# Performance work log

Measured on AMD Instinct MI355X. Metric: run time of the kernel, lower is better.

## Reference

```python
import jax, jax.numpy as jnp
import numpy as np

B, Nq, C = 1, 40000, 256
Hh, L, P = 8, 4, 8
hd = C // Hh
LEVEL_SHAPES = [(128, 128), (64, 64), (32, 32), (16, 16)]


def setup_inputs() -> dict:
    key = jax.random.key(0)
    ks = jax.random.split(key, 16)
    inp = {}
    inp['query'] = jax.random.normal(ks[0], (B, Nq, C), jnp.float32)
    # reference points in [-1, 1] normalized coords (x, y)
    inp['reference_points'] = jax.random.uniform(ks[1], (B, Nq, L, 2), jnp.float32) * 2.0 - 1.0
    for i, (h, w) in enumerate(LEVEL_SHAPES):
        inp[f'feat{i}'] = jax.random.normal(ks[2 + i], (B, C, h, w), jnp.float32)
    # learned params (torch Linear y = x @ W + b, W stored as [in, out])
    inp['W_off'] = jax.random.normal(ks[6], (C, Hh * L * P * 2), jnp.float32) * 0.02
    inp['b_off'] = jax.random.normal(ks[7], (Hh * L * P * 2,), jnp.float32) * 0.5
    inp['W_attn'] = jax.random.normal(ks[8], (C, Hh * L * P), jnp.float32) * 0.02
    inp['b_attn'] = jnp.zeros((Hh * L * P,), jnp.float32)
    inp['W_val'] = jax.random.normal(ks[9], (C, C), jnp.float32) * (1.0 / np.sqrt(C))
    inp['b_val'] = jnp.zeros((C,), jnp.float32)
    inp['W_out'] = jax.random.normal(ks[10], (C, C), jnp.float32) * (1.0 / np.sqrt(C))
    inp['b_out'] = jnp.zeros((C,), jnp.float32)
    return inp


def _deform_sample(v, coords):
    # Bilinear grid_sample, align_corners=True, zeros padding.
    # v: [B, Hh, H, W, hd]; coords: [B, Hh, S, 2] in [-1, 1] (x, y)
    _, _, H, W, _ = v.shape
    x = (coords[..., 0] + 1.0) * 0.5 * (W - 1)
    y = (coords[..., 1] + 1.0) * 0.5 * (H - 1)
    x0 = jnp.floor(x)
    y0 = jnp.floor(y)
    vflat = v.reshape(v.shape[0], v.shape[1], H * W, v.shape[4])

    def corner(xi, yi, w):
        inb = (xi >= 0) & (xi <= W - 1) & (yi >= 0) & (yi <= H - 1)
        idx = (jnp.clip(yi, 0, H - 1) * W + jnp.clip(xi, 0, W - 1)).astype(jnp.int32)
        g = jnp.take_along_axis(vflat, idx[..., None], axis=2)  # [B,Hh,S,hd]
        return g * (w * inb)[..., None]

    return (corner(x0, y0, (x0 + 1 - x) * (y0 + 1 - y))
            + corner(x0 + 1, y0, (x - x0) * (y0 + 1 - y))
            + corner(x0, y0 + 1, (x0 + 1 - x) * (y - y0))
            + corner(x0 + 1, y0 + 1, (x - x0) * (y - y0)))


def reference(query, feat0, feat1, feat2, feat3, reference_points,
              W_off, b_off, W_attn, b_attn, W_val, b_val, W_out, b_out):
    feats = [feat0, feat1, feat2, feat3]
    off = (query @ W_off + b_off).reshape(B, Nq, Hh, L, P, 2)
    w = (query @ W_attn + b_attn).reshape(B, Nq, Hh, L, P)
    w = jax.nn.softmax(w, axis=-1)  # softmax over points, per level
    # samp: [B, Nq, Hh, L, P, 2]
    samp = reference_points[:, :, None, :, None, :] + jnp.tanh(off) * 0.25

    out = jnp.zeros((B, Nq, Hh, hd), jnp.float32)
    for l, f in enumerate(feats):
        Hl, Wl = f.shape[2], f.shape[3]
        v = jnp.einsum('bchw,cd->bhwd', f, W_val) + b_val  # value proj
        v = v.reshape(B, Hl, Wl, Hh, hd).transpose(0, 3, 1, 2, 4)  # [B,Hh,H,W,hd]
        coords = samp[:, :, :, l].transpose(0, 2, 1, 3, 4).reshape(B, Hh, Nq * P, 2)
        s = _deform_sample(v, coords).reshape(B, Hh, Nq, P, hd)
        wl = w[:, :, :, l].transpose(0, 2, 1, 3)  # [B,Hh,Nq,P]
        out = out + jnp.einsum('bhnpd,bhnp->bnhd', s, wl)

    return out.reshape(B, Nq, C) @ W_out + b_out
```

## Files before the change

### kernel.cpp

```cpp
#include <hip/hip_runtime.h>
#include <hip/hip_fp16.h>
#include <math.h>

#define NQ 40000

typedef short s16x8 __attribute__((ext_vector_type(8)));
typedef float f32x4 __attribute__((ext_vector_type(4)));

static constexpr int HLa[4] = {128, 64, 32, 16};
static constexpr int HWa[4] = {16384, 4096, 1024, 256};
static constexpr int VB[4] = {0, 4194304, 5242880, 5505024};

__device__ __forceinline__ short bf16hi(float x) {
    union { float f; unsigned u; } v; v.f = x;
    unsigned r = v.u + 0x7FFFu + ((v.u >> 16) & 1u);
    return (short)(r >> 16);
}
__device__ __forceinline__ float bf16f(short s) {
    union { unsigned u; float f; } v; v.u = ((unsigned)(unsigned short)s) << 16;
    return v.f;
}
__device__ __forceinline__ float fast_tanh(float x) {
    float xc = fminf(fmaxf(x, -15.f), 15.f);
    float e = __expf(2.f * xc);
    return (e - 1.f) / (e + 1.f);
}
#define MFMA16(a, b, c) __builtin_amdgcn_mfma_f32_16x16x32_bf16(a, b, c, 0, 0, 0)

__global__ __launch_bounds__(256) void prep_w(
    const float* __restrict__ Woff, const float* __restrict__ Wattn,
    const float* __restrict__ Wout, short* __restrict__ WtH, short* __restrict__ WtL)
{
    int r = blockIdx.x, c = threadIdx.x;
    float x;
    if (r < 512)      x = Woff[c * 512 + r];
    else if (r < 768) x = Wattn[c * 256 + (r - 512)];
    else              x = Wout[c * 256 + (r - 768)];
    short hi = bf16hi(x);
    WtH[r * 256 + c] = hi;
    WtL[r * 256 + c] = bf16hi(x - bf16f(hi));
}

__global__ __launch_bounds__(256) void vproj_kernel(
    const float* __restrict__ f0, const float* __restrict__ f1,
    const float* __restrict__ f2, const float* __restrict__ f3,
    const float* __restrict__ Wv, const float* __restrict__ bv,
    __half* __restrict__ v)
{
    __shared__ float fT[256 * 16];

    int bid = blockIdx.x;
    const float* f;
    int base, HWl, hw0;
    if (bid < 1024)      { f = f0; base = VB[0]; HWl = 16384; hw0 = bid * 16; }
    else if (bid < 1280) { f = f1; base = VB[1]; HWl = 4096;  hw0 = (bid - 1024) * 16; }
    else if (bid < 1344) { f = f2; base = VB[2]; HWl = 1024;  hw0 = (bid - 1280) * 16; }
    else                 { f = f3; base = VB[3]; HWl = 256;   hw0 = (bid - 1344) * 16; }

    int t = threadIdx.x;
    for (int k = 0; k < 16; ++k) {
        int idx = k * 256 + t;
        int c = idx >> 4, j = idx & 15;
        fT[idx] = f[c * HWl + hw0 + j];
    }
    __syncthreads();

    int to4 = (t & 63) * 4;
    int hw4 = (t >> 6) * 4;

    float4 bv4 = *(const float4*)(bv + to4);
    float acc[4][4];
    #pragma unroll
    for (int i = 0; i < 4; ++i) {
        acc[i][0] = bv4.x; acc[i][1] = bv4.y; acc[i][2] = bv4.z; acc[i][3] = bv4.w;
    }

    #pragma unroll 4
    for (int c = 0; c < 256; ++c) {
        float4 w4 = *(const float4*)(Wv + c * 256 + to4);
        float4 fv = *(const float4*)(fT + c * 16 + hw4);
        float fa[4] = {fv.x, fv.y, fv.z, fv.w};
        float wa[4] = {w4.x, w4.y, w4.z, w4.w};
        #pragma unroll
        for (int i = 0; i < 4; ++i)
            #pragma unroll
            for (int j = 0; j < 4; ++j)
                acc[i][j] += fa[i] * wa[j];
    }

    int hh = to4 >> 5, dd4 = to4 & 31;
    #pragma unroll
    for (int i = 0; i < 4; ++i) {
        int hw = hw0 + hw4 + i;
        __half2 h0 = __floats2half2_rn(acc[i][0], acc[i][1]);
        __half2 h1 = __floats2half2_rn(acc[i][2], acc[i][3]);
        uint2 st = make_uint2(*(unsigned*)&h0, *(unsigned*)&h1);
        *(uint2*)(v + base + (hh * HWl + hw) * 32 + dd4) = st;
    }
}

__global__ __launch_bounds__(256, 5) void msda_kernel(
    const float* __restrict__ query, const float* __restrict__ refp,
    const float* __restrict__ boff,  const float* __restrict__ battn,
    const float* __restrict__ bout,
    const short* __restrict__ WtH,   const short* __restrict__ WtL,
    const __half* __restrict__ v,    float* __restrict__ out)
{
    __shared__ __align__(16) char lds[29952];
    short*    sQh  = (short*)lds;
    short*    sQl  = (short*)(lds + 8448);
    float*    offL = (float*)lds;
    uint2*    sPWh = (uint2*)(lds + 8448);
    __half*   sWh  = (__half*)(lds + 16896);
    unsigned* sPI  = (unsigned*)(lds + 25344);
    float*    sR   = (float*)(lds + 29440);

    const int t = threadIdx.x;
    const int n0 = blockIdx.x * 16;
    const int wv = t >> 6, lane = t & 63;
    const int mrow = lane & 15, kg = lane >> 4;

    for (int k2 = 0; k2 < 16; ++k2) {
        float x = query[(n0 + k2) * 256 + t];
        short hi = bf16hi(x);
        sQh[k2 * 264 + t] = hi;
        sQl[k2 * 264 + t] = bf16hi(x - bf16f(hi));
    }
    if (t < 128) sR[t] = refp[n0 * 8 + t];
    __syncthreads();

    f32x4 accO[8], accA[4];
    {
        f32x4 z = {0.f, 0.f, 0.f, 0.f};
        #pragma unroll
        for (int j = 0; j < 8; ++j) accO[j] = z;
        #pragma unroll
        for (int j = 0; j < 4; ++j) accA[j] = z;
    }
    {
        const short* offH = WtH + (wv * 128 + mrow) * 256 + kg * 8;
        const short* offLo = WtL + (wv * 128 + mrow) * 256 + kg * 8;
        const short* attH = WtH + (512 + wv * 64 + mrow) * 256 + kg * 8;
        const short* attL = WtL + (512 + wv * 64 + mrow) * 256 + kg * 8;
        const int aoff = mrow * 264 + kg * 8;
        #pragma unroll
        for (int kk = 0; kk < 8; ++kk) {
            s16x8 ah = *(const s16x8*)(sQh + aoff + kk * 32);
            s16x8 al = *(const s16x8*)(sQl + aoff + kk * 32);
            #pragma unroll
            for (int j = 0; j < 8; ++j) {
                s16x8 bh = *(const s16x8*)(offH + j * 4096 + kk * 32);
                s16x8 bl = *(const s16x8*)(offLo + j * 4096 + kk * 32);
                accO[j] = MFMA16(ah, bh, accO[j]);
                accO[j] = MFMA16(al, bh, accO[j]);
                accO[j] = MFMA16(ah, bl, accO[j]);
            }
            #pragma unroll
            for (int ja = 0; ja < 4; ++ja) {
                s16x8 bh = *(const s16x8*)(attH + ja * 4096 + kk * 32);
                s16x8 bl = *(const s16x8*)(attL + ja * 4096 + kk * 32);
                accA[ja] = MFMA16(ah, bh, accA[ja]);
                accA[ja] = MFMA16(al, bh, accA[ja]);
                accA[ja] = MFMA16(ah, bl, accA[ja]);
            }
        }
    }
    #pragma unroll
    for (int j = 0; j < 8; ++j) {
        float bb = boff[wv * 128 + j * 16 + mrow];
        #pragma unroll
        for (int r = 0; r < 4; ++r) accO[j][r] += bb;
    }
    #pragma unroll
    for (int ja = 0; ja < 4; ++ja) {
        float bb = battn[wv * 64 + ja * 16 + mrow];
        #pragma unroll
        for (int r = 0; r < 4; ++r) accA[ja][r] += bb;
    }

    #pragma unroll
    for (int ja = 0; ja < 4; ++ja) {
        int hh = 2 * wv + (ja >> 1);
        int l  = ((ja & 1) << 1) | (mrow >> 3);
        int p  = mrow & 7;
        #pragma unroll
        for (int r = 0; r < 4; ++r) {
            float x = accA[ja][r];
            float m = fmaxf(x, __shfl_xor(x, 1));
            m = fmaxf(m, __shfl_xor(m, 2));
            m = fmaxf(m, __shfl_xor(m, 4));
            float e = __expf(x - m);
            float s = e + __shfl_xor(e, 1);
            s += __shfl_xor(s, 2);
            s += __shfl_xor(s, 4);
            int q = kg * 4 + r;
            sWh[q * 264 + hh * 32 + l * 8 + p] = __float2half_rn(e / s);
        }
    }
    __syncthreads();

    const int dd2 = t & 15, hhpS = (t >> 4) & 1, qp = t >> 5;

    for (int k = 0; k < 4; ++k) {
        if (wv == k) {
            #pragma unroll
            for (int j = 0; j < 8; ++j)
                #pragma unroll
                for (int r = 0; r < 4; ++r)
                    offL[(kg * 4 + r) * 132 + j * 16 + mrow] = accO[j][r];
        }
        __syncthreads();

        #pragma unroll
        for (int it = 0; it < 4; ++it) {
            int s = it * 256 + t;
            int q = s >> 6, hhL = (s >> 5) & 1, l = (s >> 3) & 3, p = s & 7;
            const int Wl = 128 >> l;
            const float scl = 0.5f * (float)(Wl - 1);
            float lx = offL[q * 132 + hhL * 64 + l * 16 + p * 2];
            float ly = offL[q * 132 + hhL * 64 + l * 16 + p * 2 + 1];
            float w  = __half2float(sWh[q * 264 + (2 * k + hhL) * 32 + l * 8 + p]);
            float rx = sR[q * 8 + l * 2], ry = sR[q * 8 + l * 2 + 1];
            float cx = rx + fast_tanh(lx) * 0.25f;
            float cy = ry + fast_tanh(ly) * 0.25f;
            float xx = (cx + 1.f) * scl, yy = (cy + 1.f) * scl;
            float x0f = floorf(xx), y0f = floorf(yy);
            float fx = xx - x0f, fy = yy - y0f;
            int x0 = (int)x0f, y0 = (int)y0f;
            int xc0 = min(max(x0, 0), Wl - 1);
            int xc1 = min(max(x0 + 1, 0), Wl - 1);
            int yc0 = min(max(y0, 0), Wl - 1);
            int yc1 = min(max(y0 + 1, 0), Wl - 1);
            bool bx0 = (x0 >= 0) & (x0 < Wl);
            bool bx1 = (x0 + 1 >= 0) & (x0 + 1 < Wl);
            bool by0 = (y0 >= 0) & (y0 < Wl);
            bool by1 = (y0 + 1 >= 0) & (y0 + 1 < Wl);
            float w00 = (bx0 && by0) ? (1.f - fx) * (1.f - fy) * w : 0.f;
            float w01 = (bx1 && by0) ? fx * (1.f - fy) * w : 0.f;
            float w10 = (bx0 && by1) ? (1.f - fx) * fy * w : 0.f;
            float w11 = (bx1 && by1) ? fx * fy * w : 0.f;
            unsigned pw = (unsigned)(yc0 * Wl + xc0)
                        | ((unsigned)(xc1 - xc0) << 14)
                        | ((unsigned)(yc1 - yc0) << 15);
            sPI[s] = pw;
            __half2 hA = __floats2half2_rn(w00, w01);
            __half2 hB = __floats2half2_rn(w10, w11);
            sPWh[s] = make_uint2(*(unsigned*)&hA, *(unsigned*)&hB);
        }
        __syncthreads();

        {
            const int hh = 2 * k + hhpS;
            #pragma unroll
            for (int qi2 = 0; qi2 < 2; ++qi2) {
                int qi = qp * 2 + qi2;
                float accx = 0.f, accy = 0.f;
                #pragma unroll
                for (int l = 0; l < 4; ++l) {
                    const int Wl = HLa[l];
                    const __half2* vl = (const __half2*)(v + VB[l] + hh * HWa[l] * 32 + dd2 * 2);
                    int sbase = ((qi * 2 + hhpS) * 4 + l) * 8;
                    #pragma unroll
                    for (int p = 0; p < 8; ++p) {
                        unsigned pw = sPI[sbase + p];
                        uint2 ww = sPWh[sbase + p];
                        float2 fa = __half22float2(*(__half2*)&ww.x);
                        float2 fb = __half22float2(*(__half2*)&ww.y);
                        int idx = pw & 0x3FFF;
                        int dxo = ((pw >> 14) & 1) * 16;
                        int dyo = ((pw >> 15) & 1) * (Wl * 16);
                        const __half2* b00 = vl + idx * 16;
                        float2 f00 = __half22float2(b00[0]);
                        float2 f01 = __half22float2(b00[dxo]);
                        float2 f10 = __half22float2(b00[dyo]);
                        float2 f11 = __half22float2(b00[dxo + dyo]);
                        accx += fa.x * f00.x + fa.y * f01.x + fb.x * f10.x + fb.y * f11.x;
                        accy += fa.x * f00.y + fa.y * f01.y + fb.x * f10.y + fb.y * f11.y;
                    }
                }
                *(__half2*)(sWh + qi * 264 + hh * 32 + dd2 * 2) =
                    __floats2half2_rn(accx, accy);
            }
        }
        __syncthreads();
    }

    {
        int q = t & 15, seg = t >> 4;
        const __half2* src = (const __half2*)(sWh + q * 264 + seg * 16);
        short* dh = sQh + q * 264 + seg * 16;
        short* dl = sQl + q * 264 + seg * 16;
        #pragma unroll
        for (int jj = 0; jj < 8; ++jj) {
            float2 f = __half22float2(src[jj]);
            short h0 = bf16hi(f.x), h1 = bf16hi(f.y);
            dh[2 * jj]     = h0;
            dh[2 * jj + 1] = h1;
            dl[2 * jj]     = bf16hi(f.x - bf16f(h0));
            dl[2 * jj + 1] = bf16hi(f.y - bf16f(h1));
        }
    }
    __syncthreads();

    {
        f32x4 accE[4];
        f32x4 z = {0.f, 0.f, 0.f, 0.f};
        #pragma unroll
        for (int e = 0; e < 4; ++e) accE[e] = z;
        const short* outH = WtH + (768 + wv * 64 + mrow) * 256 + kg * 8;
        const short* outL = WtL + (768 + wv * 64 + mrow) * 256 + kg * 8;
        const int aoff = mrow * 264 + kg * 8;
        #pragma unroll
        for (int kk = 0; kk < 8; ++kk) {
            s16x8 ah = *(const s16x8*)(sQh + aoff + kk * 32);
            s16x8 al = *(const s16x8*)(sQl + aoff + kk * 32);
            #pragma unroll
            for (int e = 0; e < 4; ++e) {
                s16x8 bh = *(const s16x8*)(outH + e * 4096 + kk * 32);
                s16x8 bl = *(const s16x8*)(outL + e * 4096 + kk * 32);
                accE[e] = MFMA16(ah, bh, accE[e]);
                accE[e] = MFMA16(al, bh, accE[e]);
                accE[e] = MFMA16(ah, bl, accE[e]);
            }
        }
        #pragma unroll
        for (int e = 0; e < 4; ++e) {
            int col = wv * 64 + e * 16 + mrow;
            float bb = bout[col];
            #pragma unroll
            for (int r = 0; r < 4; ++r)
                out[(n0 + kg * 4 + r) * 256 + col] = accE[e][r] + bb;
        }
    }
}

extern "C" void kernel_launch(void* const* d_in, const int* in_sizes, int n_in,
                              void* d_out, int out_size, void* d_ws, size_t ws_size,
                              hipStream_t stream) {
    const float* query = (const float*)d_in[0];
    const float* refp  = (const float*)d_in[1];
    const float* f0    = (const float*)d_in[2];
    const float* f1    = (const float*)d_in[3];
    const float* f2    = (const float*)d_in[4];
    const float* f3    = (const float*)d_in[5];
    const float* Woff  = (const float*)d_in[6];
    const float* boff  = (const float*)d_in[7];
    const float* Wattn = (const float*)d_in[8];
    const float* battn = (const float*)d_in[9];
    const float* Wval  = (const float*)d_in[10];
    const float* bval  = (const float*)d_in[11];
    const float* Wout  = (const float*)d_in[12];
    const float* bout  = (const float*)d_in[13];

    __half* v  = (__half*)d_ws;
    short* WtH = (short*)((char*)d_ws + 11141120);
    short* WtL = WtH + 262144;
    float* outp = (float*)d_out;

    prep_w<<<1024, 256, 0, stream>>>(Woff, Wattn, Wout, WtH, WtL);
    vproj_kernel<<<1360, 256, 0, stream>>>(f0, f1, f2, f3, Wval, bval, v);
    msda_kernel<<<2500, 256, 0, stream>>>(query, refp, boff, battn, bout,
                                          WtH, WtL, v, outp);
}
```

Before: 572.2 us.

## Make sampling stage wave-local to remove block-wide barriers per head pair

Restructures the deformable sampling phase so each wave handles its own two heads across all 16 queries, using per-wave LDS scratch for offsets and sample records. This replaces the four-iteration loop with block-wide __syncthreads by wave-local lgkmcnt waits, and splits levels across lane groups with a shuffle reduction. LDS use grows from about 30KB to about 54KB, so the launch bound drops from 5 to 3 blocks per SM, which lowers occupancy for this latency-bound gather.

```diff
diff --git a/kernel.cpp b/kernel.cpp
--- a/kernel.cpp
+++ b/kernel.cpp
@@ -99,26 +99,27 @@
     }
 }
 
-__global__ __launch_bounds__(256, 5) void msda_kernel(
+__global__ __launch_bounds__(256, 3) void msda_kernel(
     const float* __restrict__ query, const float* __restrict__ refp,
     const float* __restrict__ boff,  const float* __restrict__ battn,
     const float* __restrict__ bout,
     const short* __restrict__ WtH,   const short* __restrict__ WtL,
     const __half* __restrict__ v,    float* __restrict__ out)
 {
-    __shared__ __align__(16) char lds[29952];
+    __shared__ __align__(16) char lds[54272];
     short*    sQh  = (short*)lds;
     short*    sQl  = (short*)(lds + 8448);
-    float*    offL = (float*)lds;
-    uint2*    sPWh = (uint2*)(lds + 8448);
-    __half*   sWh  = (__half*)(lds + 16896);
-    unsigned* sPI  = (unsigned*)(lds + 25344);
-    float*    sR   = (float*)(lds + 29440);
+    __half*   preT = (__half*)(lds + 33792);
+    __half*   sWh  = (__half*)(lds + 42240);
+    float*    sR   = (float*)(lds + 53760);
 
     const int t = threadIdx.x;
     const int n0 = blockIdx.x * 16;
     const int wv = t >> 6, lane = t & 63;
     const int mrow = lane & 15, kg = lane >> 4;
+    float*    offW = (float*)lds + wv * 2112;
+    unsigned* sPIw = (unsigned*)(lds + 50688 + wv * 768);
+    uint2*    sPWw = (uint2*)(lds + 50688 + wv * 768 + 256);
 
     for (int k2 = 0; k2 < 16; ++k2) {
         float x = query[(n0 + k2) * 256 + t];
@@ -177,6 +178,13 @@
         #pragma unroll
         for (int r = 0; r < 4; ++r) accA[ja][r] += bb;
     }
+    __syncthreads();
+
+    #pragma unroll
+    for (int j = 0; j < 8; ++j)
+        #pragma unroll
+        for (int r = 0; r < 4; ++r)
+            offW[(kg * 4 + r) * 132 + j * 16 + mrow] = accO[j][r];
 
     #pragma unroll
     for (int ja = 0; ja < 4; ++ja) {
@@ -197,97 +205,93 @@
             sWh[q * 264 + hh * 32 + l * 8 + p] = __float2half_rn(e / s);
         }
     }
-    __syncthreads();
-
-    const int dd2 = t & 15, hhpS = (t >> 4) & 1, qp = t >> 5;
-
-    for (int k = 0; k < 4; ++k) {
-        if (wv == k) {
-            #pragma unroll
-            for (int j = 0; j < 8; ++j)
-                #pragma unroll
-                for (int r = 0; r < 4; ++r)
-                    offL[(kg * 4 + r) * 132 + j * 16 + mrow] = accO[j][r];
-        }
-        __syncthreads();
-
-        #pragma unroll
-        for (int it = 0; it < 4; ++it) {
-            int s = it * 256 + t;
-            int q = s >> 6, hhL = (s >> 5) & 1, l = (s >> 3) & 3, p = s & 7;
-            const int Wl = 128 >> l;
-            const float scl = 0.5f * (float)(Wl - 1);
-            float lx = offL[q * 132 + hhL * 64 + l * 16 + p * 2];
-            float ly = offL[q * 132 + hhL * 64 + l * 16 + p * 2 + 1];
-            float w  = __half2float(sWh[q * 264 + (2 * k + hhL) * 32 + l * 8 + p]);
-            float rx = sR[q * 8 + l * 2], ry = sR[q * 8 + l * 2 + 1];
+    asm volatile("s_waitcnt lgkmcnt(0)" ::: "memory");
+    __builtin_amdgcn_sched_barrier(0);
+
+    const int l_p = (lane >> 3) & 3, p_p = lane & 7, hhL_p = lane >> 5;
+    const int Wl_p = 128 >> l_p;
+    const float scl_p = 0.5f * (float)(Wl_p - 1);
+    const int whCol = (2 * wv + hhL_p) * 32 + l_p * 8 + p_p;
+    const int sg = kg, ch2 = mrow;
+    const int Wl_s = 128 >> sg;
+    const int HWs = Wl_s * Wl_s;
+    const int dyoMul = Wl_s * 16;
+    const int VBs = (sg == 0) ? VB[0] : (sg == 1) ? VB[1] : (sg == 2) ? VB[2] : VB[3];
+    const __half2* vl0 = (const __half2*)(v + VBs + (2 * wv) * HWs * 32) + ch2;
+    const __half2* vl1 = (const __half2*)(v + VBs + (2 * wv + 1) * HWs * 32) + ch2;
+
+    for (int chunk = 0; chunk < 16; ++chunk) {
+        {
+            float2 ll = *(const float2*)(offW + chunk * 132 + 2 * lane);
+            float lx = ll.x, ly = ll.y;
+            float w  = __half2float(sWh[chunk * 264 + whCol]);
+            float rx = sR[chunk * 8 + l_p * 2], ry = sR[chunk * 8 + l_p * 2 + 1];
             float cx = rx + fast_tanh(lx) * 0.25f;
             float cy = ry + fast_tanh(ly) * 0.25f;
-            float xx = (cx + 1.f) * scl, yy = (cy + 1.f) * scl;
+            float xx = (cx + 1.f) * scl_p, yy = (cy + 1.f) * scl_p;
             float x0f = floorf(xx), y0f = floorf(yy);
             float fx = xx - x0f, fy = yy - y0f;
             int x0 = (int)x0f, y0 = (int)y0f;
-            int xc0 = min(max(x0, 0), Wl - 1);
-            int xc1 = min(max(x0 + 1, 0), Wl - 1);
-            int yc0 = min(max(y0, 0), Wl - 1);
-            int yc1 = min(max(y0 + 1, 0), Wl - 1);
-            bool bx0 = (x0 >= 0) & (x0 < Wl);
-            bool bx1 = (x0 + 1 >= 0) & (x0 + 1 < Wl);
-            bool by0 = (y0 >= 0) & (y0 < Wl);
-            bool by1 = (y0 + 1 >= 0) & (y0 + 1 < Wl);
+            int xc0 = min(max(x0, 0), Wl_p - 1);
+            int xc1 = min(max(x0 + 1, 0), Wl_p - 1);
+            int yc0 = min(max(y0, 0), Wl_p - 1);
+            int yc1 = min(max(y0 + 1, 0), Wl_p - 1);
+            bool bx0 = (x0 >= 0) & (x0 < Wl_p);
+            bool bx1 = (x0 + 1 >= 0) & (x0 + 1 < Wl_p);
+            bool by0 = (y0 >= 0) & (y0 < Wl_p);
+            bool by1 = (y0 + 1 >= 0) & (y0 + 1 < Wl_p);
             float w00 = (bx0 && by0) ? (1.f - fx) * (1.f - fy) * w : 0.f;
             float w01 = (bx1 && by0) ? fx * (1.f - fy) * w : 0.f;
             float w10 = (bx0 && by1) ? (1.f - fx) * fy * w : 0.f;
             float w11 = (bx1 && by1) ? fx * fy * w : 0.f;
-            unsigned pw = (unsigned)(yc0 * Wl + xc0)
+            unsigned pw = (unsigned)(yc0 * Wl_p + xc0)
                         | ((unsigned)(xc1 - xc0) << 14)
                         | ((unsigned)(yc1 - yc0) << 15);
-            sPI[s] = pw;
+            sPIw[lane] = pw;
             __half2 hA = __floats2half2_rn(w00, w01);
             __half2 hB = __floats2half2_rn(w10, w11);
-            sPWh[s] = make_uint2(*(unsigned*)&hA, *(unsigned*)&hB);
-        }
-        __syncthreads();
-
-        {
-            const int hh = 2 * k + hhpS;
-            #pragma unroll
-            for (int qi2 = 0; qi2 < 2; ++qi2) {
-                int qi = qp * 2 + qi2;
-                float accx = 0.f, accy = 0.f;
-                #pragma unroll
-                for (int l = 0; l < 4; ++l) {
-                    const int Wl = HLa[l];
-                    const __half2* vl = (const __half2*)(v + VB[l] + hh * HWa[l] * 32 + dd2 * 2);
-                    int sbase = ((qi * 2 + hhpS) * 4 + l) * 8;
-                    #pragma unroll
-                    for (int p = 0; p < 8; ++p) {
-                        unsigned pw = sPI[sbase + p];
-                        uint2 ww = sPWh[sbase + p];
-                        float2 fa = __half22float2(*(__half2*)&ww.x);
-                        float2 fb = __half22float2(*(__half2*)&ww.y);
-                        int idx = pw & 0x3FFF;
-                        int dxo = ((pw >> 14) & 1) * 16;
-                        int dyo = ((pw >> 15) & 1) * (Wl * 16);
-                        const __half2* b00 = vl + idx * 16;
-                        float2 f00 = __half22float2(b00[0]);
-                        float2 f01 = __half22float2(b00[dxo]);
-                        float2 f10 = __half22float2(b00[dyo]);
-                        float2 f11 = __half22float2(b00[dxo + dyo]);
-                        accx += fa.x * f00.x + fa.y * f01.x + fb.x * f10.x + fb.y * f11.x;
-                        accy += fa.x * f00.y + fa.y * f01.y + fb.x * f10.y + fb.y * f11.y;
-                    }
-                }
-                *(__half2*)(sWh + qi * 264 + hh * 32 + dd2 * 2) =
-                    __floats2half2_rn(accx, accy);
+            sPWw[lane] = make_uint2(*(unsigned*)&hA, *(unsigned*)&hB);
+        }
+        asm volatile("s_waitcnt lgkmcnt(0)" ::: "memory");
+        __builtin_amdgcn_sched_barrier(0);
+
+        float ax = 0.f, ay = 0.f;
+        #pragma unroll
+        for (int iter = 0; iter < 16; ++iter) {
+            const int hhL = iter >> 3, p = iter & 7;
+            const int rec = hhL * 32 + sg * 8 + p;
+            unsigned pw = sPIw[rec];
+            uint2 ww = sPWw[rec];
+            const __half2* vl = hhL ? vl1 : vl0;
+            int idx = pw & 0x3FFF;
+            int dxo = ((pw >> 14) & 1) * 16;
+            int dyo = ((pw >> 15) & 1) * dyoMul;
+            const __half2* b00 = vl + idx * 16;
+            float2 fa = __half22float2(*(__half2*)&ww.x);
+            float2 fb = __half22float2(*(__half2*)&ww.y);
+            float2 f00 = __half22float2(b00[0]);
+            float2 f01 = __half22float2(b00[dxo]);
+            float2 f10 = __half22float2(b00[dyo]);
+            float2 f11 = __half22float2(b00[dxo + dyo]);
+            ax += fa.x * f00.x + fa.y * f01.x + fb.x * f10.x + fb.y * f11.x;
+            ay += fa.x * f00.y + fa.y * f01.y + fb.x * f10.y + fb.y * f11.y;
+            if ((iter & 7) == 7) {
+                float sxv = ax + __shfl_xor(ax, 16); sxv += __shfl_xor(sxv, 32);
+                float syv = ay + __shfl_xor(ay, 16); syv += __shfl_xor(syv, 32);
+                if (sg == 0)
+                    *(__half2*)(preT + chunk * 264 + (2 * wv + hhL) * 32 + ch2 * 2) =
+                        __floats2half2_rn(sxv, syv);
+                ax = 0.f; ay = 0.f;
             }
         }
-        __syncthreads();
-    }
+        asm volatile("s_waitcnt lgkmcnt(0)" ::: "memory");
+        __builtin_amdgcn_sched_barrier(0);
+    }
+    __syncthreads();
 
     {
         int q = t & 15, seg = t >> 4;
-        const __half2* src = (const __half2*)(sWh + q * 264 + seg * 16);
+        const __half2* src = (const __half2*)(preT + q * 264 + seg * 16);
         short* dh = sQh + q * 264 + seg * 16;
         short* dl = sQl + q * 264 + seg * 16;
         #pragma unroll
```

Result: no change. 575.3 us (+0.5%).
